# Performance work log

Hardware: AMD Instinct MI355X
Metric: run time of the kernel (lower is better)

Reference implementation:

```python
import jax, jax.numpy as jnp
import numpy as np

LN_EPS = 1e-5

def setup_inputs() -> dict:
    key = jax.random.key(0)
    ks = jax.random.split(key, 7)
    B, S, P, L, D = 4, 2048, 16, 512, 1024
    # bytes in [-1, 255]; -1 marks missing bytes
    bytes_ids = jax.random.randint(ks[0], (B, S, P), 0, 257, dtype=jnp.int64) - 1
    byte_emb = jax.random.normal(ks[1], (256, L), dtype=jnp.float32) * 0.02
    pos_emb = jax.random.normal(ks[2], (P, L, L), dtype=jnp.float32) * 0.02
    up_w = jax.random.normal(ks[3], (D, L), dtype=jnp.float32) * 0.02
    up_b = jax.random.normal(ks[4], (D,), dtype=jnp.float32) * 0.02
    ln_gamma = jnp.ones((D,), dtype=jnp.float32)
    ln_beta = jnp.zeros((D,), dtype=jnp.float32)
    return {"bytes_ids": bytes_ids, "byte_emb": byte_emb, "pos_emb": pos_emb,
            "up_w": up_w, "up_b": up_b, "ln_gamma": ln_gamma, "ln_beta": ln_beta}

def reference(bytes_ids, byte_emb, pos_emb, up_w, up_b, ln_gamma, ln_beta):
    is_missing = bytes_ids == -1                      # [B,S,P]
    ids = jnp.where(is_missing, 0, bytes_ids)
    be = byte_emb[ids]                                # [B,S,P,L] gather
    # per-position matrix: 'pij,...pi->...pj'
    e = jnp.einsum('pij,bspi->bspj', pos_emb, be)     # [B,S,P,L]
    e = jnp.where(is_missing[..., None], 0.0, e)
    e = e.sum(axis=-2)                                # [B,S,L]
    e = e @ up_w.T + up_b                             # [B,S,D]
    mu = e.mean(axis=-1, keepdims=True)
    var = ((e - mu) ** 2).mean(axis=-1, keepdims=True)
    e = (e - mu) * jax.lax.rsqrt(var + LN_EPS) * ln_gamma + ln_beta
    return e
```

## Files before the change

kernel.cpp:

```cpp
#include <hip/hip_runtime.h>
#include <hip/hip_bf16.h>

#define LN_EPS 1e-5f

typedef __attribute__((ext_vector_type(8))) short short8;
typedef __attribute__((ext_vector_type(4))) float floatx4;
typedef __attribute__((ext_vector_type(4))) unsigned int uintx4;

static __device__ __forceinline__ unsigned int f2bfu(float f) {
    __hip_bfloat16 h = __float2bfloat16(f);
    return (unsigned int)__builtin_bit_cast(unsigned short, h);
}
static __device__ __forceinline__ float bf2f(unsigned short u) {
    return __builtin_bit_cast(float, (unsigned int)u << 16);
}

static __device__ __forceinline__ void gload_lds16(const void* g, void* l) {
    __builtin_amdgcn_global_load_lds(
        (const __attribute__((address_space(1))) void*)g,
        (__attribute__((address_space(3))) void*)l, 16, 0, 0);
}

#define TA_P_STRIDE (257 * 512)

__global__ __launch_bounds__(256) void k_prep(
    const float* __restrict__ up_w, const float* __restrict__ byte_emb,
    const float* __restrict__ pos_emb,
    unsigned short* __restrict__ wb, unsigned short* __restrict__ bb,
    unsigned short* __restrict__ T, unsigned short* __restrict__ PT)
{
    const int b = blockIdx.x;
    if (b < 640) {
        const float* src;
        unsigned short* dst;
        int idx;
        if (b < 512) { src = up_w;     dst = wb; idx = (b * 256 + threadIdx.x) * 4; }
        else         { src = byte_emb; dst = bb; idx = ((b - 512) * 256 + threadIdx.x) * 4; }
        const float4 v = *(const float4*)&src[idx];
        ushort4 o;
        o.x = (unsigned short)f2bfu(v.x); o.y = (unsigned short)f2bfu(v.y);
        o.z = (unsigned short)f2bfu(v.z); o.w = (unsigned short)f2bfu(v.w);
        *(ushort4*)&dst[idx] = o;
    } else if (b < 656) {
        const int p = b - 640;
        if (threadIdx.x < 128) {
            ushort4 z; z.x = z.y = z.z = z.w = 0;
            *(ushort4*)&T[(size_t)p * TA_P_STRIDE + 256 * 512 + threadIdx.x * 4] = z;
        }
    } else {
        const int idx = b - 656;
        const int j0 = (idx & 7) * 64;
        const int i0 = ((idx >> 3) & 7) * 64;
        const int p  = idx >> 6;
        const float* __restrict__ Pp = pos_emb + (size_t)p * 512 * 512;
        unsigned short* __restrict__ Tp = PT + (size_t)p * 512 * 512;

        __shared__ float S[64][65];
        const int r  = threadIdx.x >> 2;
        const int c0 = (threadIdx.x & 3) * 16;

        #pragma unroll
        for (int c = 0; c < 16; c += 4) {
            const float4 v = *(const float4*)&Pp[(size_t)(i0 + r) * 512 + j0 + c0 + c];
            S[r][c0 + c + 0] = v.x;
            S[r][c0 + c + 1] = v.y;
            S[r][c0 + c + 2] = v.z;
            S[r][c0 + c + 3] = v.w;
        }
        __syncthreads();

        #pragma unroll
        for (int h = 0; h < 2; ++h) {
            short8 o;
            #pragma unroll
            for (int k = 0; k < 8; ++k)
                o[k] = (short)f2bfu(S[c0 + h * 8 + k][r]);
            *(short8*)&Tp[(size_t)(j0 + r) * 512 + i0 + c0 + h * 8] = o;
        }
    }
}

#define GEMM_PROLOG()                                                          \
    __shared__ __align__(16) unsigned short SMEM[32768];            \
    float (*Cst)[132] = (float(*)[132])SMEM;                                   \
    const int tid = threadIdx.x;                                               \
    const int w   = tid >> 6, lane = tid & 63;                                 \
    const int lr  = lane & 15, lg = lane >> 4, lk = lg * 8;                    \
    const int wr  = w >> 1, wc = w & 1;                                        \
    const int crow = lane >> 3, ccol = (lane & 7) * 8;                         \
    floatx4 acc[4][4] = {};

#define GEMM_STAGE(b, kt) do {                                                 \
    unsigned short* Ab = SMEM + (b) * 16384;                                   \
    unsigned short* Bb = Ab + 8192;                                            \
    _Pragma("unroll")                                                          \
    for (int ci = 0; ci < 4; ++ci) {                                           \
        const int c = w + ci * 4;                                              \
        gload_lds16(&Ag[(size_t)(c * 8 + crow) * 512 + (kt) * 64 + ccol],      \
                    &Ab[c * 512]);                                             \
        gload_lds16(&Bg[(size_t)(c * 8 + crow) * 512 + (kt) * 64 + ccol],      \
                    &Bb[c * 512]);                                             \
    }                                                                          \
} while (0)

#define GEMM_COMPUTE(b) do {                                                   \
    const unsigned short* As = SMEM + (b) * 16384;                             \
    const unsigned short* Bs = As + 8192;                                      \
    _Pragma("unroll")                                                          \
    for (int kk = 0; kk < 2; ++kk) {                                           \
        short8 af[4], bf[4];                                                   \
        _Pragma("unroll")                                                      \
        for (int mf = 0; mf < 4; ++mf)                                         \
            af[mf] = *(const short8*)&As[(wr * 64 + mf * 16 + lr) * 64 + kk * 32 + lk]; \
        _Pragma("unroll")                                                      \
        for (int nf = 0; nf < 4; ++nf)                                         \
            bf[nf] = *(const short8*)&Bs[(wc * 64 + nf * 16 + lr) * 64 + kk * 32 + lk]; \
        _Pragma("unroll")                                                      \
        for (int mf = 0; mf < 4; ++mf)                                         \
            _Pragma("unroll")                                                  \
            for (int nf = 0; nf < 4; ++nf)                                     \
                acc[mf][nf] = __builtin_amdgcn_mfma_f32_16x16x32_bf16(         \
                    af[mf], bf[nf], acc[mf][nf], 0, 0, 0);                     \
    }                                                                          \
} while (0)

#define GEMM_MAIN()                                                            \
    GEMM_STAGE(0, 0);                                                          \
    __syncthreads();                                                           \
    {                                                                          \
        int buf = 0;                                                           \
        for (int kt = 0; kt < 8; ++kt) {                                       \
            if (kt < 7) GEMM_STAGE(buf ^ 1, kt + 1);                           \
            GEMM_COMPUTE(buf);                                                 \
            __syncthreads();                                                   \
            buf ^= 1;                                                          \
        }                                                                      \
    }

#define CST_STAGE(qr, addv)                                                    \
    if (wr == ((qr) >> 1)) {                                                   \
        _Pragma("unroll")                                                      \
        for (int mfq = 0; mfq < 2; ++mfq) {                                    \
            const int mf = ((qr) & 1) * 2 + mfq;                               \
            _Pragma("unroll")                                                  \
            for (int nf = 0; nf < 4; ++nf)                                     \
                _Pragma("unroll")                                              \
                for (int q = 0; q < 4; ++q)                                    \
                    Cst[mfq * 16 + lg * 4 + q][wc * 64 + nf * 16 + lr]         \
                        = acc[mf][nf][q] + addv;                               \
        }                                                                      \
    }

__global__ __launch_bounds__(256) void k1_97(
    const unsigned short* __restrict__ A,
    const unsigned short* __restrict__ PT,
    unsigned short* __restrict__ T)
{
    const int p  = blockIdx.z;
    const int n0 = blockIdx.x * 128;
    const int m0 = blockIdx.y * 128;
    const unsigned short* __restrict__ Ag = A + (size_t)m0 * 512;
    const unsigned short* __restrict__ Bg = PT + (size_t)p * 512 * 512 + (size_t)n0 * 512;
    unsigned short* __restrict__ Tp = T + (size_t)p * TA_P_STRIDE;

    GEMM_PROLOG();
    GEMM_MAIN();
    __syncthreads();

    #pragma unroll
    for (int qr = 0; qr < 4; ++qr) {
        CST_STAGE(qr, 0.0f);
        __syncthreads();
        #pragma unroll
        for (int pass = 0; pass < 2; ++pass) {
            const int row = pass * 16 + (tid >> 4);
            const int c8  = (tid & 15) * 8;
            uint4 o;
            o.x = f2bfu(Cst[row][c8 + 0]) | (f2bfu(Cst[row][c8 + 1]) << 16);
            o.y = f2bfu(Cst[row][c8 + 2]) | (f2bfu(Cst[row][c8 + 3]) << 16);
            o.z = f2bfu(Cst[row][c8 + 4]) | (f2bfu(Cst[row][c8 + 5]) << 16);
            o.w = f2bfu(Cst[row][c8 + 6]) | (f2bfu(Cst[row][c8 + 7]) << 16);
            *(uint4*)&Tp[(size_t)(m0 + qr * 32 + row) * 512 + n0 + c8] = o;
        }
        __syncthreads();
    }
}

__global__ __launch_bounds__(256) void k_up97(
    const unsigned short* __restrict__ Aep,
    const unsigned short* __restrict__ Wb,
    const float* __restrict__ up_b,
    unsigned short* __restrict__ e2)
{
    const int bid = blockIdx.y * 8 + blockIdx.x;
    const int swz = (bid & 7) * 64 + (bid >> 3);
    const int n0 = (swz & 7) * 128;
    const int m0 = (swz >> 3) * 128;
    const unsigned short* __restrict__ Ag = Aep + (size_t)m0 * 512;
    const unsigned short* __restrict__ Bg = Wb + (size_t)n0 * 512;

    GEMM_PROLOG();
    GEMM_MAIN();
    __syncthreads();

    float biasv[4];
    #pragma unroll
    for (int nf = 0; nf < 4; ++nf) biasv[nf] = up_b[n0 + wc * 64 + nf * 16 + lr];

    #pragma unroll
    for (int qr = 0; qr < 4; ++qr) {
        CST_STAGE(qr, biasv[nf]);
        __syncthreads();
        #pragma unroll
        for (int pass = 0; pass < 2; ++pass) {
            const int row = pass * 16 + (tid >> 4);
            const int c8  = (tid & 15) * 8;
            uintx4 o;
            o[0] = f2bfu(Cst[row][c8 + 0]) | (f2bfu(Cst[row][c8 + 1]) << 16);
            o[1] = f2bfu(Cst[row][c8 + 2]) | (f2bfu(Cst[row][c8 + 3]) << 16);
            o[2] = f2bfu(Cst[row][c8 + 4]) | (f2bfu(Cst[row][c8 + 5]) << 16);
            o[3] = f2bfu(Cst[row][c8 + 6]) | (f2bfu(Cst[row][c8 + 7]) << 16);
            __builtin_nontemporal_store(
                o, (uintx4*)&e2[(size_t)(m0 + qr * 32 + row) * 1024 + n0 + c8]);
        }
        __syncthreads();
    }
}

__global__ __launch_bounds__(256) void k_gather(
    const int* __restrict__ ids,
    const unsigned short* __restrict__ T,
    unsigned short* __restrict__ e_pre)
{
    const int row  = blockIdx.x * 4 + (threadIdx.x >> 6);
    const int lane = threadIdx.x & 63;
    const int* __restrict__ idr = ids + row * 16;

    float acc[8] = {};
    #pragma unroll
    for (int p = 0; p < 16; ++p) {
        const int id = idr[p];
        const unsigned int off = (unsigned int)((p * 257 + (id < 0 ? 256 : id)) * 512);
        const short8 v = *(const short8*)&T[off + lane * 8];
        #pragma unroll
        for (int j = 0; j < 8; ++j)
            acc[j] += bf2f((unsigned short)v[j]);
    }
    short8 r;
    #pragma unroll
    for (int j = 0; j < 8; ++j) r[j] = (short)f2bfu(acc[j]);
    *(short8*)&e_pre[(size_t)row * 512 + lane * 8] = r;
}

__global__ __launch_bounds__(256) void k_ln(
    const unsigned short* __restrict__ e2,
    const float* __restrict__ gamma,
    const float* __restrict__ beta,
    float* __restrict__ out)
{
    const int row = blockIdx.x;
    const int tid = threadIdx.x;

    const uint2 u = *(const uint2*)&e2[(size_t)row * 1024 + tid * 4];
    float a0 = bf2f((unsigned short)(u.x & 0xffffu));
    float a1 = bf2f((unsigned short)(u.x >> 16));
    float a2 = bf2f((unsigned short)(u.y & 0xffffu));
    float a3 = bf2f((unsigned short)(u.y >> 16));

    float s  = a0 + a1 + a2 + a3;
    float ss = a0 * a0 + a1 * a1 + a2 * a2 + a3 * a3;
    #pragma unroll
    for (int off = 32; off > 0; off >>= 1) {
        s  += __shfl_down(s,  off, 64);
        ss += __shfl_down(ss, off, 64);
    }

    __shared__ float red[8];
    const int wid = tid >> 6, lane = tid & 63;
    if (lane == 0) { red[wid] = s; red[4 + wid] = ss; }
    __syncthreads();

    const float S   = red[0] + red[1] + red[2] + red[3];
    const float SS  = red[4] + red[5] + red[6] + red[7];
    const float mu  = S * (1.0f / 1024.0f);
    const float var = SS * (1.0f / 1024.0f) - mu * mu;
    const float rstd = rsqrtf(var + LN_EPS);

    const float4 g = *(const float4*)&gamma[tid * 4];
    const float4 b = *(const float4*)&beta[tid * 4];
    floatx4 o;
    o[0] = (a0 - mu) * rstd * g.x + b.x;
    o[1] = (a1 - mu) * rstd * g.y + b.y;
    o[2] = (a2 - mu) * rstd * g.z + b.z;
    o[3] = (a3 - mu) * rstd * g.w + b.w;
    __builtin_nontemporal_store(o, (floatx4*)&out[(size_t)row * 1024 + tid * 4]);
}

extern "C" void kernel_launch(void* const* d_in, const int* in_sizes, int n_in,
                              void* d_out, int out_size, void* d_ws, size_t ws_size,
                              hipStream_t stream) {
    const int*   ids      = (const int*)d_in[0];
    const float* byte_emb = (const float*)d_in[1];
    const float* pos_emb  = (const float*)d_in[2];
    const float* up_w     = (const float*)d_in[3];
    const float* up_b     = (const float*)d_in[4];
    const float* gamma    = (const float*)d_in[5];
    const float* beta     = (const float*)d_in[6];
    float* out = (float*)d_out;

    unsigned short* wb     = (unsigned short*)d_ws;
    unsigned short* bb     = wb + (size_t)1024 * 512;
    unsigned short* posT   = bb + (size_t)256 * 512;
    unsigned short* tableA = posT + (size_t)16 * 512 * 512;
    unsigned short* e_pre  = tableA + (size_t)16 * TA_P_STRIDE;
    unsigned short* e2     = e_pre + (size_t)8192 * 512;

    const int rows = in_sizes[0] / 16;

    k_prep<<<1680, 256, 0, stream>>>(up_w, byte_emb, pos_emb, wb, bb, tableA, posT);

    dim3 g1(4, 2, 16);
    k1_97<<<g1, 256, 0, stream>>>(bb, posT, tableA);

    k_gather<<<rows / 4, 256, 0, stream>>>(ids, tableA, e_pre);

    dim3 g2(8, 64);
    k_up97<<<g2, 256, 0, stream>>>(e_pre, wb, up_b, e2);

    k_ln<<<rows, 256, 0, stream>>>(e2, gamma, beta, out);
}
```

Before: 55.37 us.

## Swizzle gather/LN blocks across XCDs, batch gather loads, cache GEMM output stores

The gather and layernorm kernels remap block indices so consecutive blocks (round-robined across the 8 XCDs) process contiguous row chunks, improving L2 locality per XCD. The gather kernel issues all 16 table loads before accumulating, giving more memory-level parallelism at the cost of more registers. The GEMM epilogue drops the nontemporal store for e2 so the intermediate can stay in cache for the following layernorm read.

```diff
diff --git a/kernel.cpp b/kernel.cpp
--- a/kernel.cpp
+++ b/kernel.cpp
@@ -215,13 +215,12 @@
         for (int pass = 0; pass < 2; ++pass) {
             const int row = pass * 16 + (tid >> 4);
             const int c8  = (tid & 15) * 8;
-            uintx4 o;
-            o[0] = f2bfu(Cst[row][c8 + 0]) | (f2bfu(Cst[row][c8 + 1]) << 16);
-            o[1] = f2bfu(Cst[row][c8 + 2]) | (f2bfu(Cst[row][c8 + 3]) << 16);
-            o[2] = f2bfu(Cst[row][c8 + 4]) | (f2bfu(Cst[row][c8 + 5]) << 16);
-            o[3] = f2bfu(Cst[row][c8 + 6]) | (f2bfu(Cst[row][c8 + 7]) << 16);
-            __builtin_nontemporal_store(
-                o, (uintx4*)&e2[(size_t)(m0 + qr * 32 + row) * 1024 + n0 + c8]);
+            uint4 o;
+            o.x = f2bfu(Cst[row][c8 + 0]) | (f2bfu(Cst[row][c8 + 1]) << 16);
+            o.y = f2bfu(Cst[row][c8 + 2]) | (f2bfu(Cst[row][c8 + 3]) << 16);
+            o.z = f2bfu(Cst[row][c8 + 4]) | (f2bfu(Cst[row][c8 + 5]) << 16);
+            o.w = f2bfu(Cst[row][c8 + 6]) | (f2bfu(Cst[row][c8 + 7]) << 16);
+            *(uint4*)&e2[(size_t)(m0 + qr * 32 + row) * 1024 + n0 + c8] = o;
         }
         __syncthreads();
     }
@@ -232,24 +231,38 @@
     const unsigned short* __restrict__ T,
     unsigned short* __restrict__ e_pre)
 {
-    const int row  = blockIdx.x * 4 + (threadIdx.x >> 6);
+    const int b    = blockIdx.x;
+    const int row  = (b & 7) * 1024 + (b >> 3) * 4 + (threadIdx.x >> 6);
     const int lane = threadIdx.x & 63;
     const int* __restrict__ idr = ids + row * 16;
 
-    float acc[8] = {};
+    uint4 u[16];
     #pragma unroll
     for (int p = 0; p < 16; ++p) {
         const int id = idr[p];
         const unsigned int off = (unsigned int)((p * 257 + (id < 0 ? 256 : id)) * 512);
-        const short8 v = *(const short8*)&T[off + lane * 8];
-        #pragma unroll
-        for (int j = 0; j < 8; ++j)
-            acc[j] += bf2f((unsigned short)v[j]);
-    }
-    short8 r;
-    #pragma unroll
-    for (int j = 0; j < 8; ++j) r[j] = (short)f2bfu(acc[j]);
-    *(short8*)&e_pre[(size_t)row * 512 + lane * 8] = r;
+        u[p] = *(const uint4*)&T[off + lane * 8];
+    }
+
+    float acc[8] = {};
+    #pragma unroll
+    for (int p = 0; p < 16; ++p) {
+        acc[0] += bf2f((unsigned short)(u[p].x & 0xffffu));
+        acc[1] += bf2f((unsigned short)(u[p].x >> 16));
+        acc[2] += bf2f((unsigned short)(u[p].y & 0xffffu));
+        acc[3] += bf2f((unsigned short)(u[p].y >> 16));
+        acc[4] += bf2f((unsigned short)(u[p].z & 0xffffu));
+        acc[5] += bf2f((unsigned short)(u[p].z >> 16));
+        acc[6] += bf2f((unsigned short)(u[p].w & 0xffffu));
+        acc[7] += bf2f((unsigned short)(u[p].w >> 16));
+    }
+
+    uint4 r;
+    r.x = f2bfu(acc[0]) | (f2bfu(acc[1]) << 16);
+    r.y = f2bfu(acc[2]) | (f2bfu(acc[3]) << 16);
+    r.z = f2bfu(acc[4]) | (f2bfu(acc[5]) << 16);
+    r.w = f2bfu(acc[6]) | (f2bfu(acc[7]) << 16);
+    *(uint4*)&e_pre[(size_t)row * 512 + lane * 8] = r;
 }
 
 __global__ __launch_bounds__(256) void k_ln(
@@ -258,7 +271,8 @@
     const float* __restrict__ beta,
     float* __restrict__ out)
 {
-    const int row = blockIdx.x;
+    const int b   = blockIdx.x;
+    const int row = (b & 7) * 1024 + (b >> 3);
     const int tid = threadIdx.x;
 
     const uint2 u = *(const uint2*)&e2[(size_t)row * 1024 + tid * 4];
@@ -287,12 +301,12 @@
     const float rstd = rsqrtf(var + LN_EPS);
 
     const float4 g = *(const float4*)&gamma[tid * 4];
-    const float4 b = *(const float4*)&beta[tid * 4];
+    const float4 bt = *(const float4*)&beta[tid * 4];
     floatx4 o;
-    o[0] = (a0 - mu) * rstd * g.x + b.x;
-    o[1] = (a1 - mu) * rstd * g.y + b.y;
-    o[2] = (a2 - mu) * rstd * g.z + b.z;
-    o[3] = (a3 - mu) * rstd * g.w + b.w;
+    o[0] = (a0 - mu) * rstd * g.x + bt.x;
+    o[1] = (a1 - mu) * rstd * g.y + bt.y;
+    o[2] = (a2 - mu) * rstd * g.z + bt.z;
+    o[3] = (a3 - mu) * rstd * g.w + bt.w;
     __builtin_nontemporal_store(o, (floatx4*)&out[(size_t)row * 1024 + tid * 4]);
 }
 
```

Measured after the change: 53.49 us. 1.04x faster.
